# Kernel tuning notes

Measured on AMD Instinct MI355X. Metric: run time of the kernel, lower is better.

## Reference

```python
import jax, jax.numpy as jnp
import numpy as np

LOG2PI = float(np.log(2.0 * np.pi))
MIN_DURATION = 1
NUM_STATES = 512
OBS_DIM = 128
B, T, K = 64, 2000, 400


def setup_inputs() -> dict:
    key = jax.random.key(0)
    ks = jax.random.split(key, 10)
    observations = jax.random.normal(ks[0], (B, T, OBS_DIM), dtype=jnp.float32)
    state_sequence = jax.random.randint(ks[1], (B, K), 0, NUM_STATES, dtype=jnp.int32)
    # durations >= min_duration so gamma log-prob stays finite
    duration_sequence = jax.random.randint(ks[2], (B, K), 1, 51, dtype=jnp.int32)
    # learned parameters, initialized as in the torch module
    alpha_params = jnp.ones((NUM_STATES,), jnp.float32)
    beta_params = jnp.ones((NUM_STATES,), jnp.float32)
    transition_logits = jax.random.normal(ks[3], (NUM_STATES, NUM_STATES), dtype=jnp.float32)
    initial_logits = jnp.zeros((NUM_STATES,), jnp.float32)
    observation_means = jax.random.normal(ks[4], (NUM_STATES, OBS_DIM), dtype=jnp.float32)
    observation_logvars = jnp.zeros((NUM_STATES, OBS_DIM), jnp.float32)
    return {
        "observations": observations,
        "alpha_params": alpha_params,
        "beta_params": beta_params,
        "transition_logits": transition_logits,
        "initial_logits": initial_logits,
        "observation_means": observation_means,
        "observation_logvars": observation_logvars,
        "state_sequence": state_sequence,
        "duration_sequence": duration_sequence,
    }


def _gamma_duration_logprob(alpha_params, beta_params, state_sequence, duration_sequence):
    # fully vectorized version of the per-sample Python loop in DurationModel
    d = duration_sequence.astype(jnp.float32)                      # [B, K]
    alpha = jax.nn.softplus(alpha_params)[state_sequence] + 1e-6   # [B, K]
    beta = jax.nn.softplus(beta_params)[state_sequence] + 1e-6
    lp = (alpha - 1.0) * jnp.log(d + 1e-8) - beta * d
    lp = lp - (jax.lax.lgamma(alpha) - alpha * jnp.log(beta))
    return jnp.where(d >= MIN_DURATION, lp, -jnp.inf)


def reference(observations, alpha_params, beta_params, transition_logits,
              initial_logits, observation_means, observation_logvars,
              state_sequence, duration_sequence):
    # --- duration log-probs per segment: [B, K]
    log_dur = _gamma_duration_logprob(alpha_params, beta_params,
                                      state_sequence, duration_sequence)

    # --- expand segments to frames: frame t belongs to segment with cum[idx-1] <= t < cum[idx]
    cum = jnp.cumsum(duration_sequence, axis=1)                    # [B, K]
    t = jnp.arange(observations.shape[1])                          # [T]
    seg_idx = jax.vmap(lambda c: jnp.searchsorted(c, t, side='right'))(cum)
    seg_idx = jnp.clip(seg_idx, 0, state_sequence.shape[1] - 1)    # [B, T]
    frame_states = jnp.take_along_axis(state_sequence, seg_idx, axis=1)  # [B, T]

    # --- diagonal-gaussian observation log-probs per frame: [B, T]
    mu = observation_means[frame_states]                           # [B, T, D]
    lv = observation_logvars[frame_states]                         # [B, T, D]
    resid2 = (observations - mu) ** 2 * jnp.exp(-lv)
    log_obs = -0.5 * jnp.sum(lv + resid2 + LOG2PI, axis=-1)        # [B, T]

    # --- initial + transition log-probs over the segment-level state chain
    log_trans = jax.nn.log_softmax(transition_logits, axis=-1)     # [S, S]
    log_init = jax.nn.log_softmax(initial_logits)                  # [S]
    trans_lp = log_trans[state_sequence[:, :-1], state_sequence[:, 1:]].sum(axis=1)  # [B]
    init_lp = log_init[state_sequence[:, 0]]                       # [B]

    # --- per-sequence supervised log-likelihood: [B]
    log_likelihood = log_obs.sum(axis=1) + log_dur.sum(axis=1) + trans_lp + init_lp
    return log_likelihood
```

## Files before the change

### kernel.cpp

```cpp
#include <hip/hip_runtime.h>
#include <hip/hip_bf16.h>
#include <math.h>

#define NS 512
#define OD 128
#define BB 64
#define TT 2000
#define KK 400
#define CHUNK 128
#define NCH 16
#define LOG2PI_F 1.8378770664093453f
#define SEQ_OFF  576
#define PART_OFF 1024


__device__ __forceinline__ float softplusf(float x) {
    return (x > 20.f) ? x : log1pf(expf(x));
}

__global__ __launch_bounds__(256) void big_kernel(
    const float* __restrict__ obs, const float* __restrict__ mu,
    const float* __restrict__ lvar, const float* __restrict__ trans,
    const float* __restrict__ init_logits,
    const float* __restrict__ alpha_p, const float* __restrict__ beta_p,
    const int* __restrict__ states, const int* __restrict__ durs,
    float* __restrict__ ws)
{
    const int tid = threadIdx.x;
    const int bid = blockIdx.x;
    __shared__ float red[4];

    if (bid < BB * NCH) {
        const int b = bid >> 4;
        const int t0 = (bid & 15) * CHUNK;

        __shared__ int fsl[CHUNK];
        __shared__ int csum[8];

        const int lane = tid & 63, w = tid >> 6;
        int s0v = 0, d0 = 0, s1v = 0, d1 = 0;
        s0v = states[b * KK + tid];
        d0  = durs[b * KK + tid];
        if (tid + 256 < KK) {
            s1v = states[b * KK + tid + 256];
            d1  = durs[b * KK + tid + 256];
        }
        int v0 = d0, v1 = d1;
        #pragma unroll
        for (int off = 1; off < 64; off <<= 1) {
            int u0 = __shfl_up(v0, off, 64);
            int u1 = __shfl_up(v1, off, 64);
            if (lane >= off) { v0 += u0; v1 += u1; }
        }
        if (lane == 63) { csum[w] = v0; csum[4 + w] = v1; }
        __syncthreads();
        int off0 = 0, off1 = 0;
        #pragma unroll
        for (int c = 0; c < 8; ++c) {
            int cs = csum[c];
            off0 += (c < w) ? cs : 0;
            off1 += (c < 4 + w) ? cs : 0;
        }
        const int c0 = v0 + off0;
        const int c1 = v1 + off1;

        {
            int a = c0 - d0, e = c0;
            a = (a < t0) ? t0 : a;
            e = (e > t0 + CHUNK) ? t0 + CHUNK : e;
            for (int t = a; t < e; ++t) fsl[t - t0] = s0v;
            int a1 = c1 - d1, e1 = (tid + 256 == KK - 1) ? t0 + CHUNK : c1;
            a1 = (a1 < t0) ? t0 : a1;
            e1 = (e1 > t0 + CHUNK) ? t0 + CHUNK : e1;
            for (int t = a1; t < e1; ++t) fsl[t - t0] = s1v;
        }
        __syncthreads();

        const int row = tid >> 5;
        const int d = (tid & 31) * 4;
        float acc = 0.f;
        if (t0 + CHUNK <= TT) {
            #pragma unroll
            for (int i = 0; i < CHUNK / 8; ++i) {
                const int t = t0 + i * 8 + row;
                const int s = fsl[i * 8 + row];
                const float4 o  = *(const float4*)(obs + ((size_t)(b * TT + t)) * OD + d);
                const float4 m  = *(const float4*)(mu  + (size_t)s * OD + d);
                const float4 lv = *(const float4*)(lvar + (size_t)s * OD + d);
                const float dx = o.x - m.x, dy = o.y - m.y, dz = o.z - m.z, dw = o.w - m.w;
                acc += lv.x + lv.y + lv.z + lv.w + 4.f * LOG2PI_F
                     + dx * dx * __expf(-lv.x) + dy * dy * __expf(-lv.y)
                     + dz * dz * __expf(-lv.z) + dw * dw * __expf(-lv.w);
            }
        } else {
            #pragma unroll
            for (int i = 0; i < CHUNK / 8; ++i) {
                const int t = t0 + i * 8 + row;
                if (t < TT) {
                    const int s = fsl[i * 8 + row];
                    const float4 o  = *(const float4*)(obs + ((size_t)(b * TT + t)) * OD + d);
                    const float4 m  = *(const float4*)(mu  + (size_t)s * OD + d);
                    const float4 lv = *(const float4*)(lvar + (size_t)s * OD + d);
                    const float dx = o.x - m.x, dy = o.y - m.y, dz = o.z - m.z, dw = o.w - m.w;
                    acc += lv.x + lv.y + lv.z + lv.w + 4.f * LOG2PI_F
                         + dx * dx * __expf(-lv.x) + dy * dy * __expf(-lv.y)
                         + dz * dz * __expf(-lv.z) + dw * dw * __expf(-lv.w);
                }
            }
        }
        for (int off = 32; off; off >>= 1) acc += __shfl_down(acc, off, 64);
        if ((tid & 63) == 0) red[tid >> 6] = acc;
        __syncthreads();
        if (tid == 0)
            ws[PART_OFF + bid] = -0.5f * (red[0] + red[1] + red[2] + red[3]);
    } else if (bid < BB * NCH + NS + 1) {
        const int r = bid - BB * NCH;
        const float* src = (r < NS) ? (trans + (size_t)r * NS) : init_logits;
        float x0 = src[tid];
        float x1 = src[tid + 256];
        float m = fmaxf(x0, x1);
        for (int off = 32; off; off >>= 1) m = fmaxf(m, __shfl_down(m, off, 64));
        if ((tid & 63) == 0) red[tid >> 6] = m;
        __syncthreads();
        m = fmaxf(fmaxf(red[0], red[1]), fmaxf(red[2], red[3]));
        __syncthreads();
        float e = __expf(x0 - m) + __expf(x1 - m);
        for (int off = 32; off; off >>= 1) e += __shfl_down(e, off, 64);
        if ((tid & 63) == 0) red[tid >> 6] = e;
        __syncthreads();
        if (tid == 0)
            ws[(r < NS) ? r : 512] = m + __logf(red[0] + red[1] + red[2] + red[3]);
    } else {
        const int b = bid - (BB * NCH + NS + 1);
        float lp = 0.f;
        for (int k = tid; k < KK; k += 256) {
            const int s = states[b * KK + k];
            const float dv = (float)durs[b * KK + k];
            const float a  = softplusf(alpha_p[s]) + 1e-6f;
            const float bt = softplusf(beta_p[s]) + 1e-6f;
            float v = (a - 1.f) * __logf(dv + 1e-8f) - bt * dv
                    + a * __logf(bt) - lgammaf(a);
            lp += (dv >= 1.f) ? v : -INFINITY;
            if (k < KK - 1)
                lp += trans[(size_t)s * NS + states[b * KK + k + 1]];
        }
        for (int off = 32; off; off >>= 1) lp += __shfl_down(lp, off, 64);
        if ((tid & 63) == 0) red[tid >> 6] = lp;
        __syncthreads();
        if (tid == 0)
            ws[SEQ_OFF + b] = red[0] + red[1] + red[2] + red[3]
                            + init_logits[states[b * KK]];
    }
}

__global__ __launch_bounds__(256) void fin_kernel(
    const int* __restrict__ states, const float* __restrict__ ws,
    float* __restrict__ out)
{
    const int b = blockIdx.x;
    const int tid = threadIdx.x;
    __shared__ float red[4];

    float lp = 0.f;
    if (tid < NCH)       lp = ws[PART_OFF + b * NCH + tid];
    else if (tid == NCH) lp = ws[SEQ_OFF + b] - ws[512];
    for (int k = tid; k < KK - 1; k += 256)
        lp -= ws[states[b * KK + k]];
    for (int off = 32; off; off >>= 1) lp += __shfl_down(lp, off, 64);
    if ((tid & 63) == 0) red[tid >> 6] = lp;
    __syncthreads();
    if (tid == 0)
        out[b] = red[0] + red[1] + red[2] + red[3];
}

extern "C" void kernel_launch(void* const* d_in, const int* in_sizes, int n_in,
                              void* d_out, int out_size, void* d_ws, size_t ws_size,
                              hipStream_t stream) {
    const float* observations = (const float*)d_in[0];
    const float* alpha_p      = (const float*)d_in[1];
    const float* beta_p       = (const float*)d_in[2];
    const float* trans        = (const float*)d_in[3];
    const float* init_logits  = (const float*)d_in[4];
    const float* obs_means    = (const float*)d_in[5];
    const float* obs_logvars  = (const float*)d_in[6];
    const int*   state_seq    = (const int*)d_in[7];
    const int*   dur_seq      = (const int*)d_in[8];

    float* ws = (float*)d_ws;
    float* out = (float*)d_out;

    big_kernel<<<BB * NCH + NS + 1 + BB, 256, 0, stream>>>(
        observations, obs_means, obs_logvars, trans, init_logits,
        alpha_p, beta_p, state_seq, dur_seq, ws);
    fin_kernel<<<BB, 256, 0, stream>>>(state_seq, ws, out);
}
```

Before: 23.27 us.

## Reorder blocks and cache per-state mean/weights across consecutive frames in obs loop

Auxiliary blocks (log-softmax rows and per-sequence duration/transition sums) are moved to the front of the grid so they are scheduled first. The observation loop changes from 8 frames per row with float4 loads to one wave per 32 consecutive frames, each lane holding 2 dims. The mean, exp(-logvar) and constant term are reloaded only when the frame's state changes, which cuts gather loads and exp calls because segments span many frames. In exchange the loop is now serial per wave and carries a software-prefetched observation load, which leaves less memory-level parallelism than the unrolled float4 version.

```diff
diff --git a/kernel.cpp b/kernel.cpp
--- a/kernel.cpp
+++ b/kernel.cpp
@@ -9,6 +9,7 @@
 #define KK 400
 #define CHUNK 128
 #define NCH 16
+#define NAUX (NS + 1 + BB)
 #define LOG2PI_F 1.8378770664093453f
 #define SEQ_OFF  576
 #define PART_OFF 1024
@@ -30,17 +31,55 @@
     const int bid = blockIdx.x;
     __shared__ float red[4];
 
-    if (bid < BB * NCH) {
-        const int b = bid >> 4;
-        const int t0 = (bid & 15) * CHUNK;
+    if (bid < NS + 1) {
+        const int r = bid;
+        const float* src = (r < NS) ? (trans + (size_t)r * NS) : init_logits;
+        float x0 = src[tid];
+        float x1 = src[tid + 256];
+        float m = fmaxf(x0, x1);
+        for (int off = 32; off; off >>= 1) m = fmaxf(m, __shfl_down(m, off, 64));
+        if ((tid & 63) == 0) red[tid >> 6] = m;
+        __syncthreads();
+        m = fmaxf(fmaxf(red[0], red[1]), fmaxf(red[2], red[3]));
+        __syncthreads();
+        float e = __expf(x0 - m) + __expf(x1 - m);
+        for (int off = 32; off; off >>= 1) e += __shfl_down(e, off, 64);
+        if ((tid & 63) == 0) red[tid >> 6] = e;
+        __syncthreads();
+        if (tid == 0)
+            ws[(r < NS) ? r : 512] = m + __logf(red[0] + red[1] + red[2] + red[3]);
+    } else if (bid < NAUX) {
+        const int b = bid - (NS + 1);
+        float lp = 0.f;
+        for (int k = tid; k < KK; k += 256) {
+            const int s = states[b * KK + k];
+            const float dv = (float)durs[b * KK + k];
+            const float a  = softplusf(alpha_p[s]) + 1e-6f;
+            const float bt = softplusf(beta_p[s]) + 1e-6f;
+            float v = (a - 1.f) * __logf(dv + 1e-8f) - bt * dv
+                    + a * __logf(bt) - lgammaf(a);
+            lp += (dv >= 1.f) ? v : -INFINITY;
+            if (k < KK - 1)
+                lp += trans[(size_t)s * NS + states[b * KK + k + 1]];
+        }
+        for (int off = 32; off; off >>= 1) lp += __shfl_down(lp, off, 64);
+        if ((tid & 63) == 0) red[tid >> 6] = lp;
+        __syncthreads();
+        if (tid == 0)
+            ws[SEQ_OFF + b] = red[0] + red[1] + red[2] + red[3]
+                            + init_logits[states[b * KK]];
+    } else {
+        const int ob = bid - NAUX;
+        const int b = ob >> 4;
+        const int t0 = (ob & 15) * CHUNK;
 
         __shared__ int fsl[CHUNK];
         __shared__ int csum[8];
 
         const int lane = tid & 63, w = tid >> 6;
-        int s0v = 0, d0 = 0, s1v = 0, d1 = 0;
-        s0v = states[b * KK + tid];
-        d0  = durs[b * KK + tid];
+        int s0v = states[b * KK + tid];
+        int d0  = durs[b * KK + tid];
+        int s1v = 0, d1 = 0;
         if (tid + 256 < KK) {
             s1v = states[b * KK + tid + 256];
             d1  = durs[b * KK + tid + 256];
@@ -76,80 +115,42 @@
         }
         __syncthreads();
 
-        const int row = tid >> 5;
-        const int d = (tid & 31) * 4;
+        const int base = w * 32;
+        const int tstart = t0 + base;
+        int nf = TT - tstart;
+        nf = (nf > 32) ? 32 : nf;
         float acc = 0.f;
-        if (t0 + CHUNK <= TT) {
-            #pragma unroll
-            for (int i = 0; i < CHUNK / 8; ++i) {
-                const int t = t0 + i * 8 + row;
-                const int s = fsl[i * 8 + row];
-                const float4 o  = *(const float4*)(obs + ((size_t)(b * TT + t)) * OD + d);
-                const float4 m  = *(const float4*)(mu  + (size_t)s * OD + d);
-                const float4 lv = *(const float4*)(lvar + (size_t)s * OD + d);
-                const float dx = o.x - m.x, dy = o.y - m.y, dz = o.z - m.z, dw = o.w - m.w;
-                acc += lv.x + lv.y + lv.z + lv.w + 4.f * LOG2PI_F
-                     + dx * dx * __expf(-lv.x) + dy * dy * __expf(-lv.y)
-                     + dz * dz * __expf(-lv.z) + dw * dw * __expf(-lv.w);
-            }
-        } else {
-            #pragma unroll
-            for (int i = 0; i < CHUNK / 8; ++i) {
-                const int t = t0 + i * 8 + row;
-                if (t < TT) {
-                    const int s = fsl[i * 8 + row];
-                    const float4 o  = *(const float4*)(obs + ((size_t)(b * TT + t)) * OD + d);
-                    const float4 m  = *(const float4*)(mu  + (size_t)s * OD + d);
-                    const float4 lv = *(const float4*)(lvar + (size_t)s * OD + d);
-                    const float dx = o.x - m.x, dy = o.y - m.y, dz = o.z - m.z, dw = o.w - m.w;
-                    acc += lv.x + lv.y + lv.z + lv.w + 4.f * LOG2PI_F
-                         + dx * dx * __expf(-lv.x) + dy * dy * __expf(-lv.y)
-                         + dz * dz * __expf(-lv.z) + dw * dw * __expf(-lv.w);
+        if (nf > 0) {
+            const float* obase = obs + ((size_t)b * TT + tstart) * OD + lane * 2;
+            int s_prev = -1;
+            float2 m2, w2;
+            float cl = 0.f;
+            int s_next = fsl[base];
+            float2 o_next = *(const float2*)(obase);
+            for (int i = 0; i < nf; ++i) {
+                const int s_cur = s_next;
+                const float2 o = o_next;
+                if (i + 1 < nf) {
+                    s_next = fsl[base + i + 1];
+                    o_next = *(const float2*)(obase + (size_t)(i + 1) * OD);
                 }
+                if (s_cur != s_prev) {
+                    s_prev = s_cur;
+                    m2 = *(const float2*)(mu + (size_t)s_cur * OD + lane * 2);
+                    const float2 lv = *(const float2*)(lvar + (size_t)s_cur * OD + lane * 2);
+                    w2.x = __expf(-lv.x);
+                    w2.y = __expf(-lv.y);
+                    cl = lv.x + lv.y + 2.f * LOG2PI_F;
+                }
+                const float dx = o.x - m2.x, dy = o.y - m2.y;
+                acc += cl + dx * dx * w2.x + dy * dy * w2.y;
             }
         }
         for (int off = 32; off; off >>= 1) acc += __shfl_down(acc, off, 64);
         if ((tid & 63) == 0) red[tid >> 6] = acc;
         __syncthreads();
         if (tid == 0)
-            ws[PART_OFF + bid] = -0.5f * (red[0] + red[1] + red[2] + red[3]);
-    } else if (bid < BB * NCH + NS + 1) {
-        const int r = bid - BB * NCH;
-        const float* src = (r < NS) ? (trans + (size_t)r * NS) : init_logits;
-        float x0 = src[tid];
-        float x1 = src[tid + 256];
-        float m = fmaxf(x0, x1);
-        for (int off = 32; off; off >>= 1) m = fmaxf(m, __shfl_down(m, off, 64));
-        if ((tid & 63) == 0) red[tid >> 6] = m;
-        __syncthreads();
-        m = fmaxf(fmaxf(red[0], red[1]), fmaxf(red[2], red[3]));
-        __syncthreads();
-        float e = __expf(x0 - m) + __expf(x1 - m);
-        for (int off = 32; off; off >>= 1) e += __shfl_down(e, off, 64);
-        if ((tid & 63) == 0) red[tid >> 6] = e;
-        __syncthreads();
-        if (tid == 0)
-            ws[(r < NS) ? r : 512] = m + __logf(red[0] + red[1] + red[2] + red[3]);
-    } else {
-        const int b = bid - (BB * NCH + NS + 1);
-        float lp = 0.f;
-        for (int k = tid; k < KK; k += 256) {
-            const int s = states[b * KK + k];
-            const float dv = (float)durs[b * KK + k];
-            const float a  = softplusf(alpha_p[s]) + 1e-6f;
-            const float bt = softplusf(beta_p[s]) + 1e-6f;
-            float v = (a - 1.f) * __logf(dv + 1e-8f) - bt * dv
-                    + a * __logf(bt) - lgammaf(a);
-            lp += (dv >= 1.f) ? v : -INFINITY;
-            if (k < KK - 1)
-                lp += trans[(size_t)s * NS + states[b * KK + k + 1]];
-        }
-        for (int off = 32; off; off >>= 1) lp += __shfl_down(lp, off, 64);
-        if ((tid & 63) == 0) red[tid >> 6] = lp;
-        __syncthreads();
-        if (tid == 0)
-            ws[SEQ_OFF + b] = red[0] + red[1] + red[2] + red[3]
-                            + init_logits[states[b * KK]];
+            ws[PART_OFF + ob] = -0.5f * (red[0] + red[1] + red[2] + red[3]);
     }
 }
 
@@ -189,7 +190,7 @@
     float* ws = (float*)d_ws;
     float* out = (float*)d_out;
 
-    big_kernel<<<BB * NCH + NS + 1 + BB, 256, 0, stream>>>(
+    big_kernel<<<NAUX + BB * NCH, 256, 0, stream>>>(
         observations, obs_means, obs_logvars, trans, init_logits,
         alpha_p, beta_p, state_seq, dur_seq, ws);
     fin_kernel<<<BB, 256, 0, stream>>>(state_seq, ws, out);
```

Result: slower. 24.89 us (+7.0%).
